# Optimization experiments

Measured on AMD Instinct MI355X. Metric: run time of the kernel, lower is better.

Reference implementation:

```python
import jax, jax.numpy as jnp
import numpy as np

B, T, D, H = 4, 2048, 1024, 16
DK = D // H

def setup_inputs() -> dict:
    key = jax.random.key(0)
    k1, k2, k3 = jax.random.split(key, 3)
    s = 1.0 / np.sqrt(D)
    return {
        "x": jax.random.normal(k1, (B, T, D), dtype=jnp.float32),
        "W_qkv": jax.random.normal(k2, (D, 3 * D), dtype=jnp.float32) * s,
        "b_qkv": jnp.zeros((3 * D,), dtype=jnp.float32),
        "W_out": jax.random.normal(k3, (D, D), dtype=jnp.float32) * s,
        "b_out": jnp.zeros((D,), dtype=jnp.float32),
    }

def reference(x, W_qkv, b_qkv, W_out, b_out):
    Bx, Tx, C = x.shape
    qkv = x @ W_qkv + b_qkv                       # [B,T,3D]
    q, k, v = jnp.split(qkv, 3, axis=-1)
    # [B,T,D] -> [B,H,T,dk]
    def heads(t):
        return t.reshape(Bx, Tx, H, DK).transpose(0, 2, 1, 3)
    q, k, v = heads(q), heads(k), heads(v)
    scores = jnp.einsum('bhqd,bhkd->bhqk', q, k) / jnp.sqrt(jnp.float32(DK))
    causal = jnp.tril(jnp.ones((Tx, Tx), dtype=bool))  # [T,T]
    scores = jnp.where(causal[None, None], scores, -jnp.inf)
    attn = jax.nn.softmax(scores, axis=-1)        # dropout p=0 (eval)
    out = jnp.einsum('bhqk,bhkd->bhqd', attn, v)  # [B,H,T,dk]
    out = out.transpose(0, 2, 1, 3).reshape(Bx, Tx, C)
    return out @ W_out + b_out
```

## Files before the change

### kernel.cpp

```cpp
#include <hip/hip_runtime.h>
#include <hip/hip_bf16.h>
#include <stdint.h>

#define T_SEQ 2048
#define DMODEL 1024
#define NH 16
#define DKH 64
#define M_TOK 8192
#define N_QKV 3072
#define K_DIM 1024

#define ATTN_SC (0.125f * 1.44269504f)

typedef __attribute__((ext_vector_type(8))) short short8;
typedef __attribute__((ext_vector_type(4))) short short4v;
typedef __attribute__((ext_vector_type(4))) float float4v;
typedef __attribute__((ext_vector_type(2))) unsigned int uint2v;

__device__ inline short bf16_bits(float f) {
  __hip_bfloat16 h = __float2bfloat16(f);
  short s;
  __builtin_memcpy(&s, &h, 2);
  return s;
}

__device__ inline short4v pack4_bf16_fast(float a, float b, float c, float d) {
  unsigned ua = __builtin_bit_cast(unsigned, a) + 0x8000u;
  unsigned ub = __builtin_bit_cast(unsigned, b) + 0x8000u;
  unsigned uc = __builtin_bit_cast(unsigned, c) + 0x8000u;
  unsigned ud = __builtin_bit_cast(unsigned, d) + 0x8000u;
  uint2v uu = {(ua >> 16) | (ub & 0xFFFF0000u),
               (uc >> 16) | (ud & 0xFFFF0000u)};
  return __builtin_bit_cast(short4v, uu);
}

__device__ inline void async_load16(const void* g, void* l) {
  __builtin_amdgcn_global_load_lds(
      (const __attribute__((address_space(1))) unsigned int*)g,
      (__attribute__((address_space(3))) unsigned int*)l,
      16, 0, 0);
}


__global__ __launch_bounds__(256) void cvt_kernel(const float* __restrict__ in,
                                                  short* __restrict__ out, int n) {
  int idx = (blockIdx.x * 256 + threadIdx.x) * 4;
  if (idx < n) {
    float4v v = *(const float4v*)(in + idx);
    short4v o;
    o[0] = bf16_bits(v[0]); o[1] = bf16_bits(v[1]);
    o[2] = bf16_bits(v[2]); o[3] = bf16_bits(v[3]);
    *(short4v*)(out + idx) = o;
  }
}

__global__ __launch_bounds__(256) void transpose_cvt(const float* __restrict__ in,
                                                     short* __restrict__ out,
                                                     int K, int N) {
  __shared__ float tile[32][33];
  int n0 = blockIdx.x * 32, k0 = blockIdx.y * 32;
  int tx = threadIdx.x, ty = threadIdx.y;
  #pragma unroll
  for (int r = ty; r < 32; r += 8)
    tile[r][tx] = in[(size_t)(k0 + r) * N + n0 + tx];
  __syncthreads();
  #pragma unroll
  for (int r = ty; r < 32; r += 8)
    out[(size_t)(n0 + r) * K + k0 + tx] = bf16_bits(tile[tx][r]);
}


template <int MODE>
__global__ __launch_bounds__(256) void gemm_bt(
    const short* __restrict__ A, const short* __restrict__ Bt,
    const float* __restrict__ bias,
    short* __restrict__ Qb, short* __restrict__ Kf, short* __restrict__ Vf,
    float* __restrict__ Cout, int M, int N, int K) {
  __shared__ __align__(16) short AsB[2][128 * 32];
  __shared__ __align__(16) short BsB[2][128 * 32];
  const int tid = threadIdx.x;
  const int lane = tid & 63;
  const int wave = tid >> 6;
  const int m0 = blockIdx.x * 128;
  const int n0 = blockIdx.y * 128;
  const int wm = (wave >> 1) * 64;
  const int wn = (wave & 1) * 64;
  const int quad = lane >> 4;
  const int l16 = lane & 15;

  float4v acc[4][4] = {};

  const int r0 = tid >> 2,        o0 = (tid & 3) * 8;
  const int r1 = (tid + 256) >> 2, o1 = ((tid + 256) & 3) * 8;
  const int lo0 = wave * 512;
  const int lo1 = 2048 + wave * 512;

  const short* Ag0 = A  + (size_t)(m0 + r0) * K + o0;
  const short* Ag1 = A  + (size_t)(m0 + r1) * K + o1;
  const short* Bg0 = Bt + (size_t)(n0 + r0) * K + o0;
  const short* Bg1 = Bt + (size_t)(n0 + r1) * K + o1;

  async_load16(Ag0, &AsB[0][0] + lo0);
  async_load16(Ag1, &AsB[0][0] + lo1);
  async_load16(Bg0, &BsB[0][0] + lo0);
  async_load16(Bg1, &BsB[0][0] + lo1);

  const int nkt = K >> 5;
  for (int it = 0; it < nkt; ++it) {
    __builtin_amdgcn_s_waitcnt(0);
    __syncthreads();

    if (it + 1 < nkt) {
      const int kt = (it + 1) << 5;
      const int nb = (it + 1) & 1;
      async_load16(Ag0 + kt, &AsB[nb][0] + lo0);
      async_load16(Ag1 + kt, &AsB[nb][0] + lo1);
      async_load16(Bg0 + kt, &BsB[nb][0] + lo0);
      async_load16(Bg1 + kt, &BsB[nb][0] + lo1);
    }

    const short* As = &AsB[it & 1][0];
    const short* Bs = &BsB[it & 1][0];
    short8 af[4], bfr[4];
    #pragma unroll
    for (int t = 0; t < 4; ++t)
      af[t] = *(const short8*)(As + (size_t)(wm + t * 16 + l16) * 32 + quad * 8);
    #pragma unroll
    for (int t = 0; t < 4; ++t)
      bfr[t] = *(const short8*)(Bs + (size_t)(wn + t * 16 + l16) * 32 + quad * 8);
    #pragma unroll
    for (int i = 0; i < 4; ++i)
      #pragma unroll
      for (int j = 0; j < 4; ++j)
        acc[i][j] = __builtin_amdgcn_mfma_f32_16x16x32_bf16(af[i], bfr[j], acc[i][j], 0, 0, 0);
  }

  if (MODE == 0) {
    #pragma unroll
    for (int tj = 0; tj < 4; ++tj) {
      int col = n0 + wn + tj * 16 + l16;
      float bz = bias[col];
      int which = col >> 10;
      int d = col & 1023;
      int h = d >> 6, dk = d & 63;
      #pragma unroll
      for (int ti = 0; ti < 4; ++ti) {
        int rbase = m0 + wm + ti * 16 + quad * 4;
        int b = rbase >> 11;
        int t = rbase & 2047;
        size_t bhoff = (size_t)(b * NH + h) * (T_SEQ * DKH);
        if (which == 2) {
          short4v pv;
          #pragma unroll
          for (int i = 0; i < 4; ++i) pv[i] = bf16_bits(acc[ti][tj][i] + bz);
          size_t off = bhoff + (size_t)(t >> 6) * 4096 +
                       ((((t >> 4) & 3) * 4 + (dk >> 4)) * 4 + ((t >> 2) & 3)) * 64 +
                       (dk & 15) * 4;
          *(short4v*)(Vf + off) = pv;
        } else if (which == 0) {
          #pragma unroll
          for (int i = 0; i < 4; ++i)
            Qb[bhoff + (size_t)(t + i) * DKH + dk] =
                bf16_bits((acc[ti][tj][i] + bz) * ATTN_SC);
        } else {
          int h2 = dk >> 5, qd = (dk >> 3) & 3, w = dk & 7;
          size_t kbase = bhoff + (size_t)(t >> 6) * 4096 +
                         ((((t >> 4) & 3) * 2 + h2) * 4 + qd) * 128 + w;
          int lb = t & 15;
          #pragma unroll
          for (int i = 0; i < 4; ++i)
            Kf[kbase + (lb + i) * 8] = bf16_bits(acc[ti][tj][i] + bz);
        }
      }
    }
  } else {
    #pragma unroll
    for (int tj = 0; tj < 4; ++tj) {
      int col = n0 + wn + tj * 16 + l16;
      float bz = bias[col];
      #pragma unroll
      for (int ti = 0; ti < 4; ++ti)
        #pragma unroll
        for (int i = 0; i < 4; ++i) {
          int row = m0 + wm + ti * 16 + quad * 4 + i;
          Cout[(size_t)row * N + col] = acc[ti][tj][i] + bz;
        }
    }
  }
}


template <int MASK>
__device__ __forceinline__ void attn_tile(
    const short* __restrict__ Ks, const short* __restrict__ Vs,
    const short8 aq[2][2], short4v ones,
    float4v oc[2][4], float4v lc[2],
    int dkq, int quad, int l16) {
  const int mb = dkq + quad * 4 - l16;
  #pragma unroll
  for (int c = 0; c < 4; ++c) {
    short8 b0 = *(const short8*)(Ks + (c * 2 + 0) * 512 + quad * 128 + l16 * 8);
    short8 b1 = *(const short8*)(Ks + (c * 2 + 1) * 512 + quad * 128 + l16 * 8);
    short4v vf[4];
    #pragma unroll
    for (int d = 0; d < 4; ++d)
      vf[d] = *(const short4v*)(Vs + (c * 4 + d) * 256 + quad * 64 + l16 * 4);
    #pragma unroll
    for (int qi = 0; qi < 2; ++qi) {
      float4v z = {0.f, 0.f, 0.f, 0.f};
      z = __builtin_amdgcn_mfma_f32_16x16x32_bf16(b0, aq[qi][0], z, 0, 0, 0);
      z = __builtin_amdgcn_mfma_f32_16x16x32_bf16(b1, aq[qi][1], z, 0, 0, 0);
      float p[4];
      #pragma unroll
      for (int i = 0; i < 4; ++i) {
        p[i] = __builtin_amdgcn_exp2f(z[i]);
        if (MASK && (mb + c * 16 + i - qi * 16 > 0)) p[i] = 0.f;
      }
      short4v pb = pack4_bf16_fast(p[0], p[1], p[2], p[3]);
      lc[qi] = __builtin_amdgcn_mfma_f32_16x16x16bf16_1k(ones, pb, lc[qi], 0, 0, 0);
      #pragma unroll
      for (int d = 0; d < 4; ++d)
        oc[qi][d] = __builtin_amdgcn_mfma_f32_16x16x16bf16_1k(vf[d], pb, oc[qi][d], 0, 0, 0);
    }
  }
}

__global__ __launch_bounds__(256) void attn_kernel(const short* __restrict__ Qb,
                                                   const short* __restrict__ Kf,
                                                   const short* __restrict__ Vf,
                                                   short* __restrict__ Ao) {
  __shared__ __align__(16) short KsB[2][4096];
  __shared__ __align__(16) short VsB[2][4096];
  const int bh = blockIdx.x;
  const int qb = 15 - blockIdx.y;
  const int tid = threadIdx.x;
  const int lane = tid & 63, wave = tid >> 6;
  const int quad = lane >> 4, l16 = lane & 15;
  const int qw0 = qb * 128 + wave * 32;
  const int nkb = 2 * qb + 2;

  const short* Qg = Qb + ((size_t)bh * T_SEQ + qw0) * DKH;
  const short* Kg0 = Kf + (size_t)bh * (T_SEQ * DKH);
  const short* Vg0 = Vf + (size_t)bh * (T_SEQ * DKH);

  short8 aq[2][2];
  #pragma unroll
  for (int qi = 0; qi < 2; ++qi)
    #pragma unroll
    for (int h = 0; h < 2; ++h)
      aq[qi][h] = *(const short8*)(Qg + (size_t)(qi * 16 + l16) * DKH + h * 32 + quad * 8);

  float4v oc[2][4] = {};
  float4v lc[2] = {};
  short4v ones = {0x3F80, 0x3F80, 0x3F80, 0x3F80};

  async_load16(Kg0 + tid * 8,        &KsB[0][0] + wave * 512);
  async_load16(Kg0 + 2048 + tid * 8, &KsB[0][0] + 2048 + wave * 512);
  async_load16(Vg0 + tid * 8,        &VsB[0][0] + wave * 512);
  async_load16(Vg0 + 2048 + tid * 8, &VsB[0][0] + 2048 + wave * 512);

  for (int kb = 0; kb < nkb; ++kb) {
    __builtin_amdgcn_s_waitcnt(0);
    __syncthreads();

    if (kb + 1 < nkb) {
      const int nb = (kb + 1) & 1;
      const short* Kg = Kg0 + (size_t)(kb + 1) * 4096;
      const short* Vg = Vg0 + (size_t)(kb + 1) * 4096;
      async_load16(Kg + tid * 8,        &KsB[nb][0] + wave * 512);
      async_load16(Kg + 2048 + tid * 8, &KsB[nb][0] + 2048 + wave * 512);
      async_load16(Vg + tid * 8,        &VsB[nb][0] + wave * 512);
      async_load16(Vg + 2048 + tid * 8, &VsB[nb][0] + 2048 + wave * 512);
    }

    const int dkq = kb * 64 - qw0;
    if (dkq + 63 <= 0) {
      attn_tile<0>(&KsB[kb & 1][0], &VsB[kb & 1][0], aq, ones, oc, lc, dkq, quad, l16);
    } else if (dkq <= 31) {
      attn_tile<1>(&KsB[kb & 1][0], &VsB[kb & 1][0], aq, ones, oc, lc, dkq, quad, l16);
    }
  }

  const int b = bh >> 4, h = bh & 15;
  #pragma unroll
  for (int qi = 0; qi < 2; ++qi) {
    float rl = 1.0f / lc[qi][0];
    #pragma unroll
    for (int d = 0; d < 4; ++d) {
      short4v o;
      #pragma unroll
      for (int i = 0; i < 4; ++i) o[i] = bf16_bits(oc[qi][d][i] * rl);
      int t = qw0 + qi * 16 + l16;
      *(short4v*)(Ao + (size_t)(b * T_SEQ + t) * DMODEL + h * DKH + d * 16 + quad * 4) = o;
    }
  }
}


extern "C" void kernel_launch(void* const* d_in, const int* in_sizes, int n_in,
                              void* d_out, int out_size, void* d_ws, size_t ws_size,
                              hipStream_t stream) {
  const float* x    = (const float*)d_in[0];
  const float* Wqkv = (const float*)d_in[1];
  const float* bqkv = (const float*)d_in[2];
  const float* Wout = (const float*)d_in[3];
  const float* bout = (const float*)d_in[4];
  float* out = (float*)d_out;

  char* ws = (char*)d_ws;
  short* Xb    = (short*)(ws);
  short* Wqkvt = (short*)(ws + (16ull << 20));
  short* Woutt = (short*)(ws + (22ull << 20));
  short* Qb    = (short*)(ws + (24ull << 20));
  short* Kf    = (short*)(ws + (40ull << 20));
  short* Vf    = (short*)(ws + (56ull << 20));
  short* Ao    = (short*)(ws + (72ull << 20));

  cvt_kernel<<<(M_TOK * K_DIM / 4 + 255) / 256, 256, 0, stream>>>(x, Xb, M_TOK * K_DIM);
  dim3 tb(32, 8);
  transpose_cvt<<<dim3(N_QKV / 32, K_DIM / 32), tb, 0, stream>>>(Wqkv, Wqkvt, K_DIM, N_QKV);
  transpose_cvt<<<dim3(DMODEL / 32, K_DIM / 32), tb, 0, stream>>>(Wout, Woutt, K_DIM, DMODEL);

  gemm_bt<0><<<dim3(M_TOK / 128, N_QKV / 128), 256, 0, stream>>>(
      Xb, Wqkvt, bqkv, Qb, Kf, Vf, nullptr, M_TOK, N_QKV, K_DIM);

  attn_kernel<<<dim3(64, T_SEQ / 128), 256, 0, stream>>>(Qb, Kf, Vf, Ao);

  gemm_bt<1><<<dim3(M_TOK / 128, DMODEL / 128), 256, 0, stream>>>(
      Ao, Woutt, bout, nullptr, nullptr, nullptr, out, M_TOK, DMODEL, K_DIM);
}
```

Measured before the change: 257.9 us.

## Swizzle GEMM LDS layout and transpose MFMA outputs for vectorized epilogue stores

Adds an XOR-style swizzle to the global-to-LDS load offsets and the matching LDS fragment reads, to cut shared-memory bank conflicts in the GEMM. For the Q/K and output GEMMs it swaps the MFMA operand order so each lane holds four consecutive columns. That lets the epilogue write short4/float4 vectors and load bias as float4, replacing scalar scattered stores. The QKV GEMM is split into two launches (Q/K and V) so each has its own specialized epilogue, at the cost of an extra kernel launch.

```diff
diff --git a/kernel.cpp b/kernel.cpp
--- a/kernel.cpp
+++ b/kernel.cpp
@@ -70,19 +70,20 @@
 }
 
 
-template <int MODE>
+template <int EPI>
 __global__ __launch_bounds__(256) void gemm_bt(
     const short* __restrict__ A, const short* __restrict__ Bt,
     const float* __restrict__ bias,
     short* __restrict__ Qb, short* __restrict__ Kf, short* __restrict__ Vf,
-    float* __restrict__ Cout, int M, int N, int K) {
+    float* __restrict__ Cout, int M, int N, int K, int ntile0) {
+  constexpr bool CT = (EPI != 1);
   __shared__ __align__(16) short AsB[2][128 * 32];
   __shared__ __align__(16) short BsB[2][128 * 32];
   const int tid = threadIdx.x;
   const int lane = tid & 63;
   const int wave = tid >> 6;
   const int m0 = blockIdx.x * 128;
-  const int n0 = blockIdx.y * 128;
+  const int n0 = (blockIdx.y + ntile0) * 128;
   const int wm = (wave >> 1) * 64;
   const int wn = (wave & 1) * 64;
   const int quad = lane >> 4;
@@ -90,15 +91,17 @@
 
   float4v acc[4][4] = {};
 
-  const int r0 = tid >> 2,        o0 = (tid & 3) * 8;
-  const int r1 = (tid + 256) >> 2, o1 = ((tid + 256) & 3) * 8;
+  const int r0 = tid >> 2, r1 = r0 + 64;
+  const int oswz = (((tid & 3) - (tid >> 3)) & 3) * 8;
   const int lo0 = wave * 512;
   const int lo1 = 2048 + wave * 512;
 
-  const short* Ag0 = A  + (size_t)(m0 + r0) * K + o0;
-  const short* Ag1 = A  + (size_t)(m0 + r1) * K + o1;
-  const short* Bg0 = Bt + (size_t)(n0 + r0) * K + o0;
-  const short* Bg1 = Bt + (size_t)(n0 + r1) * K + o1;
+  const short* Ag0 = A  + (size_t)(m0 + r0) * K + oswz;
+  const short* Ag1 = A  + (size_t)(m0 + r1) * K + oswz;
+  const short* Bg0 = Bt + (size_t)(n0 + r0) * K + oswz;
+  const short* Bg1 = Bt + (size_t)(n0 + r1) * K + oswz;
+
+  const int sw = ((quad + (l16 >> 1)) & 3) * 8;
 
   async_load16(Ag0, &AsB[0][0] + lo0);
   async_load16(Ag1, &AsB[0][0] + lo1);
@@ -124,67 +127,80 @@
     short8 af[4], bfr[4];
     #pragma unroll
     for (int t = 0; t < 4; ++t)
-      af[t] = *(const short8*)(As + (size_t)(wm + t * 16 + l16) * 32 + quad * 8);
+      af[t] = *(const short8*)(As + (size_t)(wm + t * 16 + l16) * 32 + sw);
     #pragma unroll
     for (int t = 0; t < 4; ++t)
-      bfr[t] = *(const short8*)(Bs + (size_t)(wn + t * 16 + l16) * 32 + quad * 8);
+      bfr[t] = *(const short8*)(Bs + (size_t)(wn + t * 16 + l16) * 32 + sw);
     #pragma unroll
     for (int i = 0; i < 4; ++i)
       #pragma unroll
-      for (int j = 0; j < 4; ++j)
-        acc[i][j] = __builtin_amdgcn_mfma_f32_16x16x32_bf16(af[i], bfr[j], acc[i][j], 0, 0, 0);
-  }
-
-  if (MODE == 0) {
+      for (int j = 0; j < 4; ++j) {
+        if (CT)
+          acc[i][j] = __builtin_amdgcn_mfma_f32_16x16x32_bf16(bfr[j], af[i], acc[i][j], 0, 0, 0);
+        else
+          acc[i][j] = __builtin_amdgcn_mfma_f32_16x16x32_bf16(af[i], bfr[j], acc[i][j], 0, 0, 0);
+      }
+  }
+
+  if (EPI == 0) {
+    const int which = n0 >> 10;
     #pragma unroll
     for (int tj = 0; tj < 4; ++tj) {
-      int col = n0 + wn + tj * 16 + l16;
-      float bz = bias[col];
-      int which = col >> 10;
-      int d = col & 1023;
-      int h = d >> 6, dk = d & 63;
+      const int colb = n0 + wn + tj * 16 + quad * 4;
+      float4v bz = *(const float4v*)(bias + colb);
+      const int d = colb & 1023;
+      const int h = d >> 6, dkb = d & 63;
       #pragma unroll
       for (int ti = 0; ti < 4; ++ti) {
-        int rbase = m0 + wm + ti * 16 + quad * 4;
-        int b = rbase >> 11;
-        int t = rbase & 2047;
-        size_t bhoff = (size_t)(b * NH + h) * (T_SEQ * DKH);
-        if (which == 2) {
-          short4v pv;
-          #pragma unroll
-          for (int i = 0; i < 4; ++i) pv[i] = bf16_bits(acc[ti][tj][i] + bz);
-          size_t off = bhoff + (size_t)(t >> 6) * 4096 +
-                       ((((t >> 4) & 3) * 4 + (dk >> 4)) * 4 + ((t >> 2) & 3)) * 64 +
-                       (dk & 15) * 4;
-          *(short4v*)(Vf + off) = pv;
-        } else if (which == 0) {
-          #pragma unroll
-          for (int i = 0; i < 4; ++i)
-            Qb[bhoff + (size_t)(t + i) * DKH + dk] =
-                bf16_bits((acc[ti][tj][i] + bz) * ATTN_SC);
+        const int tok = m0 + wm + ti * 16 + l16;
+        const int b = tok >> 11, t = tok & 2047;
+        const size_t bhoff = (size_t)(b * NH + h) * (T_SEQ * DKH);
+        float4v v = acc[ti][tj];
+        if (which == 0) {
+          short4v o = pack4_bf16_fast((v[0] + bz[0]) * ATTN_SC, (v[1] + bz[1]) * ATTN_SC,
+                                      (v[2] + bz[2]) * ATTN_SC, (v[3] + bz[3]) * ATTN_SC);
+          *(short4v*)(Qb + bhoff + (size_t)t * DKH + dkb) = o;
         } else {
-          int h2 = dk >> 5, qd = (dk >> 3) & 3, w = dk & 7;
+          short4v o = pack4_bf16_fast(v[0] + bz[0], v[1] + bz[1], v[2] + bz[2], v[3] + bz[3]);
+          const int h2 = dkb >> 5, qd = (dkb >> 3) & 3, w = dkb & 7;
           size_t kbase = bhoff + (size_t)(t >> 6) * 4096 +
-                         ((((t >> 4) & 3) * 2 + h2) * 4 + qd) * 128 + w;
-          int lb = t & 15;
-          #pragma unroll
-          for (int i = 0; i < 4; ++i)
-            Kf[kbase + (lb + i) * 8] = bf16_bits(acc[ti][tj][i] + bz);
+                         ((((t >> 4) & 3) * 2 + h2) * 4 + qd) * 128 + (t & 15) * 8 + w;
+          *(short4v*)(Kf + kbase) = o;
         }
       }
     }
+  } else if (EPI == 1) {
+    #pragma unroll
+    for (int tj = 0; tj < 4; ++tj) {
+      const int col = n0 + wn + tj * 16 + l16;
+      const float bz = bias[col];
+      const int d = col & 1023;
+      const int h = d >> 6, dk = d & 63;
+      #pragma unroll
+      for (int ti = 0; ti < 4; ++ti) {
+        const int rbase = m0 + wm + ti * 16 + quad * 4;
+        const int b = rbase >> 11, t = rbase & 2047;
+        const size_t bhoff = (size_t)(b * NH + h) * (T_SEQ * DKH);
+        float4v v = acc[ti][tj];
+        short4v pv = pack4_bf16_fast(v[0] + bz, v[1] + bz, v[2] + bz, v[3] + bz);
+        size_t off = bhoff + (size_t)(t >> 6) * 4096 +
+                     ((((t >> 4) & 3) * 4 + (dk >> 4)) * 4 + ((t >> 2) & 3)) * 64 +
+                     (dk & 15) * 4;
+        *(short4v*)(Vf + off) = pv;
+      }
+    }
   } else {
     #pragma unroll
     for (int tj = 0; tj < 4; ++tj) {
-      int col = n0 + wn + tj * 16 + l16;
-      float bz = bias[col];
-      #pragma unroll
-      for (int ti = 0; ti < 4; ++ti)
-        #pragma unroll
-        for (int i = 0; i < 4; ++i) {
-          int row = m0 + wm + ti * 16 + quad * 4 + i;
-          Cout[(size_t)row * N + col] = acc[ti][tj][i] + bz;
-        }
+      const int colb = n0 + wn + tj * 16 + quad * 4;
+      float4v bz = *(const float4v*)(bias + colb);
+      #pragma unroll
+      for (int ti = 0; ti < 4; ++ti) {
+        const int row = m0 + wm + ti * 16 + l16;
+        float4v v = acc[ti][tj];
+        float4v o = {v[0] + bz[0], v[1] + bz[1], v[2] + bz[2], v[3] + bz[3]};
+        *(float4v*)(Cout + (size_t)row * N + colb) = o;
+      }
     }
   }
 }
@@ -321,11 +337,13 @@
   transpose_cvt<<<dim3(N_QKV / 32, K_DIM / 32), tb, 0, stream>>>(Wqkv, Wqkvt, K_DIM, N_QKV);
   transpose_cvt<<<dim3(DMODEL / 32, K_DIM / 32), tb, 0, stream>>>(Wout, Woutt, K_DIM, DMODEL);
 
-  gemm_bt<0><<<dim3(M_TOK / 128, N_QKV / 128), 256, 0, stream>>>(
-      Xb, Wqkvt, bqkv, Qb, Kf, Vf, nullptr, M_TOK, N_QKV, K_DIM);
+  gemm_bt<0><<<dim3(M_TOK / 128, 16), 256, 0, stream>>>(
+      Xb, Wqkvt, bqkv, Qb, Kf, nullptr, nullptr, M_TOK, N_QKV, K_DIM, 0);
+  gemm_bt<1><<<dim3(M_TOK / 128, 8), 256, 0, stream>>>(
+      Xb, Wqkvt, bqkv, nullptr, nullptr, Vf, nullptr, M_TOK, N_QKV, K_DIM, 16);
 
   attn_kernel<<<dim3(64, T_SEQ / 128), 256, 0, stream>>>(Qb, Kf, Vf, Ao);
 
-  gemm_bt<1><<<dim3(M_TOK / 128, DMODEL / 128), 256, 0, stream>>>(
-      Ao, Woutt, bout, nullptr, nullptr, nullptr, out, M_TOK, DMODEL, K_DIM);
-}
+  gemm_bt<2><<<dim3(M_TOK / 128, DMODEL / 128), 256, 0, stream>>>(
+      Ao, Woutt, bout, nullptr, nullptr, nullptr, out, M_TOK, DMODEL, K_DIM, 0);
+}
```

New measurement: 252.8 us. 1.02x faster.
